# Optimization experiments

Measured on AMD Instinct MI355X. Metric: run time of the kernel, lower is better.

## Reference

```python
import jax, jax.numpy as jnp
import numpy as np

N_NODES = 50000
N_EDGES = 800000
N_FEATS = 128
E_FEATS = 64
N_OUT = 64
E_OUT = 32
HID = 128  # num_hids = [128]; f lifts node features to this dim
N_STEPS = 3


def _mlp(v, W1, b1, W2, b2):
    # one hidden ReLU layer, linear output (same structure for all 7 transforms)
    return jax.nn.relu(v @ W1 + b1) @ W2 + b2


def _init_mlp(key, d_in, d_hid, d_out, scale=0.05):
    k1, k2 = jax.random.split(key)
    return (jax.random.normal(k1, (d_in, d_hid), jnp.float32) * scale,
            jnp.zeros((d_hid,), jnp.float32),
            jax.random.normal(k2, (d_hid, d_out), jnp.float32) * scale,
            jnp.zeros((d_out,), jnp.float32))


def setup_inputs() -> dict:
    key = jax.random.key(0)
    ks = jax.random.split(key, 10)
    x = jax.random.normal(ks[0], (N_NODES, N_FEATS), jnp.float32)
    xe = jax.random.normal(ks[1], (N_EDGES, E_FEATS), jnp.float32)
    edge_index = jax.random.randint(ks[2], (2, N_EDGES), 0, N_NODES, jnp.int32)
    inp = {"x": x, "xe": xe, "edge_index": edge_index}
    names = ["f", "g", "h", "k1", "k2", "k", "l"]
    dims = {"f": (N_FEATS, HID), "g": (HID, HID), "h": (HID, N_OUT),
            "k1": (HID, HID), "k2": (HID, HID), "k": (E_FEATS, HID), "l": (HID, E_OUT)}
    for i, nm in enumerate(names):
        d_in, d_out = dims[nm]
        W1, b1, W2, b2 = _init_mlp(ks[3 + i], d_in, HID, d_out)
        inp[nm + "_W1"], inp[nm + "_b1"] = W1, b1
        inp[nm + "_W2"], inp[nm + "_b2"] = W2, b2
    return inp


def reference(x, xe, edge_index,
              f_W1, f_b1, f_W2, f_b2,
              g_W1, g_b1, g_W2, g_b2,
              h_W1, h_b1, h_W2, h_b2,
              k1_W1, k1_b1, k1_W2, k1_b2,
              k2_W1, k2_b1, k2_W2, k2_b2,
              k_W1, k_b1, k_W2, k_b2,
              l_W1, l_b1, l_W2, l_b2):
    src, dst = edge_index[0], edge_index[1]
    # 1. y = f(x): lift node features to HID
    y = _mlp(x, f_W1, f_b1, f_W2, f_b2)
    # 2. message passing: y <- g(sum over neighbors of y) + y
    for _ in range(N_STEPS):
        agg = jax.ops.segment_sum(y[src], dst, num_segments=N_NODES)  # [N, HID]
        y = _mlp(agg, g_W1, g_b1, g_W2, g_b2) + y
    # 3. node output z = h(y)
    node_out = _mlp(y, h_W1, h_b1, h_W2, h_b2)  # [N, N_OUT]
    # 4. edge output z_ij = l(k1(y_i) + k2(y_j) + k(x_ij))
    e_hid = (_mlp(y[src], k1_W1, k1_b1, k1_W2, k1_b2)
             + _mlp(y[dst], k2_W1, k2_b1, k2_W2, k2_b2)
             + _mlp(xe, k_W1, k_b1, k_W2, k_b2))  # [E, HID]
    edge_out = _mlp(e_hid, l_W1, l_b1, l_W2, l_b2)  # [E, E_OUT]
    return node_out, edge_out
```

## Files before the change

### kernel.cpp

```cpp
#include <hip/hip_runtime.h>
#include <hip/hip_bf16.h>

namespace {

constexpr int NN = 50000;
constexpr int NE = 800000;

typedef __attribute__((ext_vector_type(8))) short bf16x8;
typedef __attribute__((ext_vector_type(4))) float f32x4;

__device__ __forceinline__ short f2bf(float f) {
  union { __hip_bfloat16 h; short s; } u;
  u.h = __float2bfloat16(f);
  return u.s;
}
__device__ __forceinline__ float bf2f(short s) {
  union { unsigned int u; float f; } v;
  v.u = ((unsigned int)(unsigned short)s) << 16;
  return v.f;
}
__device__ __forceinline__ unsigned int pkbf2(float a, float b) {
  return (unsigned int)(unsigned short)f2bf(a) |
         ((unsigned int)(unsigned short)f2bf(b) << 16);
}

struct WTab {
  const float* W[14];
  short* out[14];
  int din[14];
  int dout[14];
};

__global__ __launch_bounds__(256) void wfrag_all(WTab tab) {
  int wi = blockIdx.y;
  int din = tab.din[wi], dout = tab.dout[wi];
  int total = din * dout;
  int gid = blockIdx.x * 256 + threadIdx.x;
  if (gid >= total) return;
  const float* W = tab.W[wi];
  short* Wf = tab.out[wi];
  int j = gid & 7;
  int l = (gid >> 3) & 63;
  int rest = gid >> 9;
  int nK = din >> 5;
  int kc = rest % nK;
  int t = rest / nK;
  int n = t * 16 + (l & 15);
  int k = kc * 32 + (l >> 4) * 8 + j;
  Wf[gid] = f2bf(W[(size_t)k * dout + n]);
}

__global__ __launch_bounds__(256) void hist_kernel(const int* __restrict__ edst,
                                                   int* __restrict__ deg) {
  int e = blockIdx.x * 256 + threadIdx.x;
  if (e < NE) atomicAdd(&deg[edst[e]], 1);
}

__global__ __launch_bounds__(256) void scan1_kernel(const int* __restrict__ deg,
                                                    int* __restrict__ excl,
                                                    int* __restrict__ bsum, int N) {
  __shared__ int s[256];
  int tid = threadIdx.x;
  int i = blockIdx.x * 256 + tid;
  int v = (i < N) ? deg[i] : 0;
  s[tid] = v;
  __syncthreads();
  for (int d = 1; d < 256; d <<= 1) {
    int t = (tid >= d) ? s[tid - d] : 0;
    __syncthreads();
    s[tid] += t;
    __syncthreads();
  }
  if (i < N) excl[i] = s[tid] - v;
  if (tid == 255) bsum[blockIdx.x] = s[255];
}

__global__ __launch_bounds__(256) void scan2_kernel(const int* __restrict__ bsum,
                                                    int* __restrict__ boff, int nb) {
  __shared__ int s[256];
  int tid = threadIdx.x;
  int v = (tid < nb) ? bsum[tid] : 0;
  s[tid] = v;
  __syncthreads();
  for (int d = 1; d < 256; d <<= 1) {
    int t = (tid >= d) ? s[tid - d] : 0;
    __syncthreads();
    s[tid] += t;
    __syncthreads();
  }
  if (tid <= nb) boff[tid] = s[tid] - v;
}

__global__ __launch_bounds__(256) void scan3_kernel(const int* __restrict__ excl,
                                                    const int* __restrict__ boff,
                                                    int* __restrict__ row_start,
                                                    int N, int nb) {
  int i = blockIdx.x * 256 + threadIdx.x;
  if (i < N) row_start[i] = excl[i] + boff[i >> 8];
  else if (i == N) row_start[N] = boff[nb];
}

__global__ __launch_bounds__(256) void fill_kernel(const int* __restrict__ esrc,
                                                   const int* __restrict__ edst,
                                                   const int* __restrict__ row_start,
                                                   int* __restrict__ cursor,
                                                   int* __restrict__ adj) {
  int e = blockIdx.x * 256 + threadIdx.x;
  if (e >= NE) return;
  int d = edst[e];
  int p = atomicAdd(&cursor[d], 1);
  adj[row_start[d] + p] = esrc[e];
}

__global__ __launch_bounds__(256) void agg_kernel(const ushort* __restrict__ yb,
                                                  const int* __restrict__ row_start,
                                                  const int* __restrict__ adj,
                                                  ushort* __restrict__ aggb) {
  int gid = blockIdx.x * 256 + threadIdx.x;
  int lane = gid & 63;
  int g = lane >> 4;
  int q = lane & 15;
  int n = (gid >> 6) * 4 + g;
  int s0 = row_start[n], s1 = row_start[n + 1];
  float a0 = 0, a1 = 0, a2 = 0, a3 = 0, a4 = 0, a5 = 0, a6 = 0, a7 = 0;
  for (int base = s0; base < s1; base += 16) {
    int idx = 0;
    if (base + q < s1) idx = adj[base + q];
    int cnt = s1 - base;
    if (cnt > 16) cnt = 16;
#pragma unroll
    for (int j = 0; j < 16; ++j) {
      if (j < cnt) {
        int s = __shfl(idx, g * 16 + j);
        uint4 v = *reinterpret_cast<const uint4*>(yb + (size_t)s * 128 + q * 8);
        a0 += bf2f((short)(v.x & 0xffff)); a1 += bf2f((short)(v.x >> 16));
        a2 += bf2f((short)(v.y & 0xffff)); a3 += bf2f((short)(v.y >> 16));
        a4 += bf2f((short)(v.z & 0xffff)); a5 += bf2f((short)(v.z >> 16));
        a6 += bf2f((short)(v.w & 0xffff)); a7 += bf2f((short)(v.w >> 16));
      }
    }
  }
  uint4 o;
  o.x = pkbf2(a0, a1);
  o.y = pkbf2(a2, a3);
  o.z = pkbf2(a4, a5);
  o.w = pkbf2(a6, a7);
  *reinterpret_cast<uint4*>(aggb + (size_t)n * 128 + q * 8) = o;
}


template <int NG, int NTHR>
__device__ __forceinline__ void wcopy(short* dst, const short* __restrict__ src,
                                      int tid) {
#pragma unroll
  for (int g0 = 0; g0 < NG; g0 += NTHR) {
    int g = g0 + tid;
    if (g < NG)
      *reinterpret_cast<bf16x8*>(dst + (size_t)g * 8) =
          *reinterpret_cast<const bf16x8*>(src + (size_t)g * 8);
  }
}

template <int KCPH, int NT>
__device__ __forceinline__ void gemm16(const char* tb, const short* wbuf,
                                       int rbase, int lane, f32x4 (&acc)[NT]) {
#pragma unroll
  for (int kc = 0; kc < KCPH; ++kc) {
    int row = rbase + (lane & 15);
    int off = (row * 256 + kc * 64 + (lane >> 4) * 16) ^ ((row & 7) << 4);
    bf16x8 a = *reinterpret_cast<const bf16x8*>(tb + off);
    __builtin_amdgcn_s_setprio(1);
#pragma unroll
    for (int t = 0; t < NT; ++t) {
      bf16x8 b = *reinterpret_cast<const bf16x8*>(wbuf + ((size_t)((t * KCPH + kc) * 64 + lane)) * 8);
      acc[t] = __builtin_amdgcn_mfma_f32_16x16x32_bf16(a, b, acc[t], 0, 0, 0);
    }
    __builtin_amdgcn_s_setprio(0);
  }
}

template <int NT>
__device__ __forceinline__ void zero16(f32x4 (&acc)[NT]) {
  const f32x4 vzero = {0.f, 0.f, 0.f, 0.f};
#pragma unroll
  for (int t = 0; t < NT; ++t) acc[t] = vzero;
}

template <int NT, bool RELU>
__device__ __forceinline__ void epi16(char* dst, int rbase, int lane,
                                      const float* bias, f32x4 (&acc)[NT]) {
#pragma unroll
  for (int t = 0; t < NT; ++t) {
    int col = t * 16 + (lane & 15);
    float bb = bias[col];
#pragma unroll
    for (int i = 0; i < 4; ++i) {
      int row = rbase + (lane >> 4) * 4 + i;
      float h = acc[t][i] + bb;
      if (RELU) h = fmaxf(h, 0.f);
      int off = (row * 256 + col * 2) ^ ((row & 7) << 4);
      *reinterpret_cast<short*>(dst + off) = f2bf(h);
    }
  }
}

template <bool INBF16, bool SKIP, bool WY>
__global__ __launch_bounds__(1024, 1) void mlp_big(
    const void* __restrict__ Xv,
    const short* __restrict__ W1f, const float* __restrict__ b1,
    const short* __restrict__ W2f, const float* __restrict__ b2,
    float* __restrict__ y, ushort* __restrict__ bfout, int nrows) {
  __shared__ alignas(16) short tile_[256 * 128];
  __shared__ alignas(16) short wb1[16384];
  __shared__ alignas(16) short wb2[16384];
  char* tb = reinterpret_cast<char*>(tile_);
  const int tid = threadIdx.x;
  const int lane = tid & 63;
  const int wave = tid >> 6;
  const int row0 = blockIdx.x * 256;
  const int wbase = wave * 16;

  wcopy<2048, 1024>(wb1, W1f, tid);
  wcopy<2048, 1024>(wb2, W2f, tid);
  __syncthreads();

  if constexpr (INBF16) {
    const ushort* X = (const ushort*)Xv;
#pragma unroll
    for (int it = 0; it < 4; ++it) {
      int idx = it * 64 + lane;
      int r = wbase + (idx >> 4);
      int c = idx & 15;
      int gr = row0 + r;
      bf16x8 v = {};
      if (gr < nrows) v = *reinterpret_cast<const bf16x8*>(X + (size_t)gr * 128 + c * 8);
      int off = (r * 256 + c * 16) ^ ((r & 7) << 4);
      *reinterpret_cast<bf16x8*>(tb + off) = v;
    }
  } else {
    const float* X = (const float*)Xv;
#pragma unroll
    for (int it = 0; it < 8; ++it) {
      int idx = it * 64 + lane;
      int r = wbase + (idx >> 5);
      int c = idx & 31;
      int gr = row0 + r;
      float4 v = make_float4(0.f, 0.f, 0.f, 0.f);
      if (gr < nrows) v = *reinterpret_cast<const float4*>(X + (size_t)gr * 128 + c * 4);
      short4 p;
      p.x = f2bf(v.x); p.y = f2bf(v.y); p.z = f2bf(v.z); p.w = f2bf(v.w);
      int off = (r * 256 + c * 8) ^ ((r & 7) << 4);
      *reinterpret_cast<short4*>(tb + off) = p;
    }
  }

  f32x4 acc[8];
  zero16(acc);
  gemm16<4, 8>(tb, wb1, wbase, lane, acc);
  epi16<8, true>(tb, wbase, lane, b1, acc);

  f32x4 acc2[8];
  zero16(acc2);
  gemm16<4, 8>(tb, wb2, wbase, lane, acc2);

#pragma unroll
  for (int t = 0; t < 8; ++t) {
    int col = t * 16 + (lane & 15);
    float bb = b2[col];
#pragma unroll
    for (int i = 0; i < 4; ++i) {
      int row = wbase + (lane >> 4) * 4 + i;
      int gr = row0 + row;
      if (gr < nrows) {
        float v = acc2[t][i] + bb;
        if constexpr (SKIP) v += y[(size_t)gr * 128 + col];
        if constexpr (WY) y[(size_t)gr * 128 + col] = v;
        int off = (row * 256 + col * 2) ^ ((row & 7) << 4);
        *reinterpret_cast<short*>(tb + off) = f2bf(v);
      }
    }
  }
#pragma unroll
  for (int rr = 0; rr < 16; ++rr) {
    int row = wbase + rr;
    int gr = row0 + row;
    if (gr < nrows) {
      int off = (row * 256 + lane * 4) ^ ((row & 7) << 4);
      unsigned int v = *reinterpret_cast<const unsigned int*>(tb + off);
      *reinterpret_cast<unsigned int*>(bfout + (size_t)gr * 128 + lane * 2) = v;
    }
  }
}

__global__ __launch_bounds__(1024, 1) void mlp_tail3(
    const ushort* __restrict__ X,
    const short* __restrict__ k1W1f, const float* __restrict__ k1b1,
    const short* __restrict__ k1W2f, const float* __restrict__ k1b2,
    const short* __restrict__ k2W1f, const float* __restrict__ k2b1,
    const short* __restrict__ k2W2f, const float* __restrict__ k2b2,
    const short* __restrict__ hW1f, const float* __restrict__ hb1,
    const short* __restrict__ hW2f, const float* __restrict__ hb2,
    ushort* __restrict__ u1b, ushort* __restrict__ u2b,
    float* __restrict__ node_out, int nrows) {
  __shared__ alignas(16) short tile_[256 * 128];
  __shared__ alignas(16) short wb1[16384];
  __shared__ alignas(16) short wb2[16384];
  char* tb = reinterpret_cast<char*>(tile_);
  const int tid = threadIdx.x;
  const int lane = tid & 63;
  const int wave = tid >> 6;
  const int row0 = blockIdx.x * 256;
  const int wbase = wave * 16;
  const int mode = blockIdx.y;

  const short* W1f = (mode == 0) ? k1W1f : (mode == 1) ? k2W1f : hW1f;
  const float* b1 = (mode == 0) ? k1b1 : (mode == 1) ? k2b1 : hb1;
  const short* W2f = (mode == 0) ? k1W2f : (mode == 1) ? k2W2f : hW2f;
  const float* b2 = (mode == 0) ? k1b2 : (mode == 1) ? k2b2 : hb2;

  wcopy<2048, 1024>(wb1, W1f, tid);
  if (mode < 2) wcopy<2048, 1024>(wb2, W2f, tid);
  else wcopy<1024, 1024>(wb2, W2f, tid);
  __syncthreads();

#pragma unroll
  for (int it = 0; it < 4; ++it) {
    int idx = it * 64 + lane;
    int r = wbase + (idx >> 4);
    int c = idx & 15;
    int gr = row0 + r;
    bf16x8 v = {};
    if (gr < nrows) v = *reinterpret_cast<const bf16x8*>(X + (size_t)gr * 128 + c * 8);
    int off = (r * 256 + c * 16) ^ ((r & 7) << 4);
    *reinterpret_cast<bf16x8*>(tb + off) = v;
  }

  f32x4 acc[8];
  zero16(acc);
  gemm16<4, 8>(tb, wb1, wbase, lane, acc);
  epi16<8, true>(tb, wbase, lane, b1, acc);

  if (mode < 2) {
    f32x4 acc2[8];
    zero16(acc2);
    gemm16<4, 8>(tb, wb2, wbase, lane, acc2);
    epi16<8, false>(tb, wbase, lane, b2, acc2);
    ushort* ub = (mode == 0) ? u1b : u2b;
#pragma unroll
    for (int rr = 0; rr < 16; ++rr) {
      int row = wbase + rr;
      int gr = row0 + row;
      if (gr < nrows) {
        int off = (row * 256 + lane * 4) ^ ((row & 7) << 4);
        unsigned int v = *reinterpret_cast<const unsigned int*>(tb + off);
        *reinterpret_cast<unsigned int*>(ub + (size_t)gr * 128 + lane * 2) = v;
      }
    }
  } else {
    f32x4 acc2[4];
    zero16(acc2);
    gemm16<4, 4>(tb, wb2, wbase, lane, acc2);
#pragma unroll
    for (int t = 0; t < 4; ++t) {
      int col = t * 16 + (lane & 15);
      float bb = b2[col];
#pragma unroll
      for (int i = 0; i < 4; ++i) {
        int row = wbase + (lane >> 4) * 4 + i;
        int gr = row0 + row;
        if (gr < nrows) node_out[(size_t)gr * 64 + col] = acc2[t][i] + bb;
      }
    }
  }
}

__global__ __launch_bounds__(1024, 1) void edge_kernel(
    const float* __restrict__ xe, const int* __restrict__ esrc,
    const int* __restrict__ edst, const ushort* __restrict__ u1b,
    const ushort* __restrict__ u2b,
    const short* __restrict__ kW1f, const float* __restrict__ kb1,
    const short* __restrict__ kW2f, const float* __restrict__ kb2,
    const short* __restrict__ lW1f, const float* __restrict__ lb1,
    const short* __restrict__ lW2f, const float* __restrict__ lb2,
    float* __restrict__ out) {
  __shared__ alignas(16) short wK1[8192];
  __shared__ alignas(16) short wK2[16384];
  __shared__ alignas(16) short wL1[16384];
  __shared__ alignas(16) short wL2[4096];
  __shared__ alignas(16) short tile_[256 * 128];
  __shared__ float biasL[416];
  char* tb = reinterpret_cast<char*>(tile_);
  const int tid = threadIdx.x;
  const int lane = tid & 63;
  const int wave = tid >> 6;
  const int f4 = lane & 31;
  const int hs = lane >> 5;
  const int wbase = wave * 16;

  wcopy<1024, 1024>(wK1, kW1f, tid);
  wcopy<2048, 1024>(wK2, kW2f, tid);
  wcopy<2048, 1024>(wL1, lW1f, tid);
  wcopy<512, 1024>(wL2, lW2f, tid);
  if (tid < 128) biasL[tid] = kb1[tid];
  else if (tid < 256) biasL[tid] = kb2[tid - 128];
  else if (tid < 384) biasL[tid] = lb1[tid - 256];
  else if (tid < 416) biasL[tid] = lb2[tid - 384];
  __syncthreads();

  constexpr int NTILES = NE / 256;

  for (int tile = blockIdx.x; tile < NTILES; tile += gridDim.x) {
    const int ebase = tile * 256 + wbase;

    const int vcur = (lane < 32) ? esrc[ebase + (lane & 15)] : edst[ebase + (lane & 15)];

#pragma unroll
    for (int i = 0; i < 4; ++i) {
      int idx = i * 64 + lane;
      int r = idx >> 4, c = idx & 15;
      float4 v = *reinterpret_cast<const float4*>(xe + (size_t)(ebase + r) * 64 + c * 4);
      short4 p;
      p.x = f2bf(v.x); p.y = f2bf(v.y);
      p.z = f2bf(v.z); p.w = f2bf(v.w);
      int rr = wbase + r;
      int off = (rr * 256 + c * 8) ^ ((rr & 7) << 4);
      *reinterpret_cast<short4*>(tb + off) = p;
    }

    ushort4 ga[4], gb[4];
#pragma unroll
    for (int i = 0; i < 4; ++i) {
      int s = __shfl(vcur, i * 2 + hs);
      int d = __shfl(vcur, 32 + i * 2 + hs);
      ga[i] = *reinterpret_cast<const ushort4*>(u1b + (size_t)s * 128 + f4 * 4);
      gb[i] = *reinterpret_cast<const ushort4*>(u2b + (size_t)d * 128 + f4 * 4);
    }

    f32x4 acc[8];
    zero16(acc);
    gemm16<2, 8>(tb, wK1, wbase, lane, acc);
    epi16<8, true>(tb, wbase, lane, &biasL[0], acc);

    ushort4 ga2[4], gb2[4];
#pragma unroll
    for (int i = 0; i < 4; ++i) {
      int s = __shfl(vcur, (4 + i) * 2 + hs);
      int d = __shfl(vcur, 32 + (4 + i) * 2 + hs);
      ga2[i] = *reinterpret_cast<const ushort4*>(u1b + (size_t)s * 128 + f4 * 4);
      gb2[i] = *reinterpret_cast<const ushort4*>(u2b + (size_t)d * 128 + f4 * 4);
    }
    uint2 gsum[8];
#pragma unroll
    for (int i = 0; i < 4; ++i) {
      float s0 = bf2f((short)ga[i].x) + bf2f((short)gb[i].x);
      float s1 = bf2f((short)ga[i].y) + bf2f((short)gb[i].y);
      float s2 = bf2f((short)ga[i].z) + bf2f((short)gb[i].z);
      float s3 = bf2f((short)ga[i].w) + bf2f((short)gb[i].w);
      gsum[i] = make_uint2(pkbf2(s0, s1), pkbf2(s2, s3));
    }

    zero16(acc);
    gemm16<4, 8>(tb, wK2, wbase, lane, acc);
    epi16<8, false>(tb, wbase, lane, &biasL[128], acc);

#pragma unroll
    for (int i = 0; i < 4; ++i) {
      float s0 = bf2f((short)ga2[i].x) + bf2f((short)gb2[i].x);
      float s1 = bf2f((short)ga2[i].y) + bf2f((short)gb2[i].y);
      float s2 = bf2f((short)ga2[i].z) + bf2f((short)gb2[i].z);
      float s3 = bf2f((short)ga2[i].w) + bf2f((short)gb2[i].w);
      gsum[4 + i] = make_uint2(pkbf2(s0, s1), pkbf2(s2, s3));
    }

#pragma unroll
    for (int i = 0; i < 8; ++i) {
      int r = wbase + i * 2 + hs;
      int off = (r * 256 + f4 * 8) ^ ((r & 7) << 4);
      short4 c = *reinterpret_cast<short4*>(tb + off);
      uint2 g = gsum[i];
      short4 nw;
      nw.x = f2bf(bf2f(c.x) + bf2f((short)(g.x & 0xffff)));
      nw.y = f2bf(bf2f(c.y) + bf2f((short)(g.x >> 16)));
      nw.z = f2bf(bf2f(c.z) + bf2f((short)(g.y & 0xffff)));
      nw.w = f2bf(bf2f(c.w) + bf2f((short)(g.y >> 16)));
      *reinterpret_cast<short4*>(tb + off) = nw;
    }

    zero16(acc);
    gemm16<4, 8>(tb, wL1, wbase, lane, acc);
    epi16<8, true>(tb, wbase, lane, &biasL[256], acc);

    f32x4 acc4[2];
    zero16(acc4);
    gemm16<4, 2>(tb, wL2, wbase, lane, acc4);

#pragma unroll
    for (int t = 0; t < 2; ++t) {
      int col = t * 16 + (lane & 15);
      float bb = biasL[384 + col];
#pragma unroll
      for (int i = 0; i < 4; ++i) {
        int row = (lane >> 4) * 4 + i;
        out[(size_t)(ebase + row) * 32 + col] = acc4[t][i] + bb;
      }
    }
  }
}

}

extern "C" void kernel_launch(void* const* d_in, const int* in_sizes, int n_in,
                              void* d_out, int out_size, void* d_ws, size_t ws_size,
                              hipStream_t stream) {
  const float* x = (const float*)d_in[0];
  const float* xe = (const float*)d_in[1];
  const int* eidx = (const int*)d_in[2];
  const int* esrc = eidx;
  const int* edst = eidx + NE;

  const float* fb1 = (const float*)d_in[4];
  const float* fb2 = (const float*)d_in[6];
  const float* gb1 = (const float*)d_in[8];
  const float* gb2 = (const float*)d_in[10];
  const float* hb1 = (const float*)d_in[12];
  const float* hb2 = (const float*)d_in[14];
  const float* k1b1 = (const float*)d_in[16];
  const float* k1b2 = (const float*)d_in[18];
  const float* k2b1 = (const float*)d_in[20];
  const float* k2b2 = (const float*)d_in[22];
  const float* kb1 = (const float*)d_in[24];
  const float* kb2 = (const float*)d_in[26];
  const float* lb1 = (const float*)d_in[28];
  const float* lb2 = (const float*)d_in[30];

  char* ws = (char*)d_ws;
  size_t off = 0;
  auto alloc = [&](size_t bytes) -> void* {
    void* p = ws + off;
    off = (off + bytes + 255) & ~(size_t)255;
    return p;
  };
  float* y = (float*)alloc((size_t)NN * 128 * 4);
  ushort* ybA = (ushort*)alloc((size_t)NN * 128 * 2);
  ushort* ybB = (ushort*)alloc((size_t)NN * 128 * 2);
  ushort* aggb = (ushort*)alloc((size_t)NN * 128 * 2);
  ushort* u1b = (ushort*)alloc((size_t)NN * 128 * 2);
  ushort* u2b = (ushort*)alloc((size_t)NN * 128 * 2);
  int* deg = (int*)alloc((size_t)NN * 4);
  int* excl = (int*)alloc((size_t)NN * 4);
  int* bsum = (int*)alloc(256 * 4);
  int* boff = (int*)alloc(256 * 4);
  int* row_start = (int*)alloc((size_t)(NN + 16) * 4);
  int* cursor = (int*)alloc((size_t)NN * 4);
  int* adj = (int*)alloc((size_t)NE * 4);

  const int wi[14] = {3, 5, 7, 9, 11, 13, 15, 17, 19, 21, 23, 25, 27, 29};
  const int wdin[14] = {128, 128, 128, 128, 128, 128, 128, 128, 128, 128, 64, 128, 128, 128};
  const int wdout[14] = {128, 128, 128, 128, 128, 64, 128, 128, 128, 128, 128, 128, 128, 32};
  WTab tab;
  short* wf[14];
  for (int i = 0; i < 14; ++i) {
    size_t elems = (size_t)wdin[i] * wdout[i];
    wf[i] = (short*)alloc(elems * 2);
    tab.W[i] = (const float*)d_in[wi[i]];
    tab.out[i] = wf[i];
    tab.din[i] = wdin[i];
    tab.dout[i] = wdout[i];
  }
  wfrag_all<<<dim3(64, 14, 1), 256, 0, stream>>>(tab);

  short* fW1f = wf[0];  short* fW2f = wf[1];
  short* gW1f = wf[2];  short* gW2f = wf[3];
  short* hW1f = wf[4];  short* hW2f = wf[5];
  short* k1W1f = wf[6]; short* k1W2f = wf[7];
  short* k2W1f = wf[8]; short* k2W2f = wf[9];
  short* kW1f = wf[10]; short* kW2f = wf[11];
  short* lW1f = wf[12]; short* lW2f = wf[13];

  const int nb = (NN + 255) / 256;
  hipMemsetAsync(deg, 0, (size_t)NN * 4, stream);
  hist_kernel<<<(NE + 255) / 256, 256, 0, stream>>>(edst, deg);
  scan1_kernel<<<nb, 256, 0, stream>>>(deg, excl, bsum, NN);
  scan2_kernel<<<1, 256, 0, stream>>>(bsum, boff, nb);
  scan3_kernel<<<(NN + 256) / 256 + 1, 256, 0, stream>>>(excl, boff, row_start, NN, nb);
  hipMemsetAsync(cursor, 0, (size_t)NN * 4, stream);
  fill_kernel<<<(NE + 255) / 256, 256, 0, stream>>>(esrc, edst, row_start, cursor, adj);

  const int nblk = (NN + 255) / 256;

  mlp_big<false, false, true><<<nblk, 1024, 0, stream>>>(
      x, fW1f, fb1, fW2f, fb2, y, ybA, NN);

  ushort* ybin = ybA;
  ushort* ybout = ybB;
  for (int s = 0; s < 3; ++s) {
    agg_kernel<<<(NN / 4 * 64) / 256, 256, 0, stream>>>(ybin, row_start, adj, aggb);
    mlp_big<true, true, true><<<nblk, 1024, 0, stream>>>(
        aggb, gW1f, gb1, gW2f, gb2, y, ybout, NN);
    ushort* t = ybin; ybin = ybout; ybout = t;
  }

  mlp_tail3<<<dim3(nblk, 3), 1024, 0, stream>>>(
      ybin, k1W1f, k1b1, k1W2f, k1b2, k2W1f, k2b1, k2W2f, k2b2,
      hW1f, hb1, hW2f, hb2, u1b, u2b, (float*)d_out, NN);

  float* edge_out = (float*)d_out + (size_t)NN * 64;
  edge_kernel<<<256, 1024, 0, stream>>>(xe, esrc, edst, u1b, u2b, kW1f, kb1, kW2f, kb2,
                                        lW1f, lb1, lW2f, lb2, edge_out);
}
```

Before: 504.6 us.

## Prefetch next edge tile into registers and stage output through LDS

Each wave now loads the next tile's edge indices and xe features into registers during the L1 GEMM of the current tile, hiding global load latency behind compute. The edge output is first written to the wave's own LDS tile region and then stored to global memory as coalesced float2 rows instead of scattered scalar stores. This raises register pressure (16 extra floats plus an index) in a kernel with launch bounds of 1024 threads, which could cause spills. It also reuses the tile LDS area without extra sync, relying on the region being wave-private.

```diff
diff --git a/kernel.cpp b/kernel.cpp
--- a/kernel.cpp
+++ b/kernel.cpp
@@ -371,6 +371,20 @@
         if (gr < nrows) node_out[(size_t)gr * 64 + col] = acc2[t][i] + bb;
       }
     }
+  }
+}
+
+__device__ __forceinline__ void load_tile_regs(const float* __restrict__ xe,
+                                               const int* __restrict__ esrc,
+                                               const int* __restrict__ edst,
+                                               int ebase, int lane,
+                                               int& vint, float4 (&xr)[4]) {
+  vint = (lane < 32) ? esrc[ebase + (lane & 15)] : edst[ebase + (lane & 15)];
+#pragma unroll
+  for (int i = 0; i < 4; ++i) {
+    int idx = i * 64 + lane;
+    int r = idx >> 4, c = idx & 15;
+    xr[i] = *reinterpret_cast<const float4*>(xe + (size_t)(ebase + r) * 64 + c * 4);
   }
 }
 
@@ -396,6 +410,7 @@
   const int f4 = lane & 31;
   const int hs = lane >> 5;
   const int wbase = wave * 16;
+  char* myA = tb + wbase * 256;
 
   wcopy<1024, 1024>(wK1, kW1f, tid);
   wcopy<2048, 1024>(wK2, kW2f, tid);
@@ -408,20 +423,22 @@
   __syncthreads();
 
   constexpr int NTILES = NE / 256;
-
-  for (int tile = blockIdx.x; tile < NTILES; tile += gridDim.x) {
+  int tile = blockIdx.x;
+  int vnext;
+  float4 xr[4];
+  load_tile_regs(xe, esrc, edst, tile * 256 + wbase, lane, vnext, xr);
+
+  for (; tile < NTILES; tile += gridDim.x) {
     const int ebase = tile * 256 + wbase;
-
-    const int vcur = (lane < 32) ? esrc[ebase + (lane & 15)] : edst[ebase + (lane & 15)];
+    const int vcur = vnext;
 
 #pragma unroll
     for (int i = 0; i < 4; ++i) {
       int idx = i * 64 + lane;
       int r = idx >> 4, c = idx & 15;
-      float4 v = *reinterpret_cast<const float4*>(xe + (size_t)(ebase + r) * 64 + c * 4);
       short4 p;
-      p.x = f2bf(v.x); p.y = f2bf(v.y);
-      p.z = f2bf(v.z); p.w = f2bf(v.w);
+      p.x = f2bf(xr[i].x); p.y = f2bf(xr[i].y);
+      p.z = f2bf(xr[i].z); p.w = f2bf(xr[i].w);
       int rr = wbase + r;
       int off = (rr * 256 + c * 8) ^ ((rr & 7) << 4);
       *reinterpret_cast<short4*>(tb + off) = p;
@@ -486,6 +503,10 @@
       *reinterpret_cast<short4*>(tb + off) = nw;
     }
 
+    int nt2 = tile + gridDim.x;
+    if (nt2 < NTILES)
+      load_tile_regs(xe, esrc, edst, nt2 * 256 + wbase, lane, vnext, xr);
+
     zero16(acc);
     gemm16<4, 8>(tb, wL1, wbase, lane, acc);
     epi16<8, true>(tb, wbase, lane, &biasL[256], acc);
@@ -501,8 +522,14 @@
 #pragma unroll
       for (int i = 0; i < 4; ++i) {
         int row = (lane >> 4) * 4 + i;
-        out[(size_t)(ebase + row) * 32 + col] = acc4[t][i] + bb;
+        *reinterpret_cast<float*>(myA + row * 128 + col * 4) = acc4[t][i] + bb;
       }
+    }
+#pragma unroll
+    for (int it = 0; it < 4; ++it) {
+      int r = it * 4 + (lane >> 4);
+      float2 v = *reinterpret_cast<const float2*>(myA + r * 128 + (lane & 15) * 8);
+      *reinterpret_cast<float2*>(out + (size_t)(ebase + r) * 32 + (lane & 15) * 2) = v;
     }
   }
 }
```

Measured after the change: 580.2 us. 1.15x slower.
